# Kernel optimization log

Measured on AMD Instinct MI355X. Metric: run time of the kernel, lower is better.

## Reference

```python
import jax, jax.numpy as jnp
import numpy as np
import math

D_MODEL = 1024
D_HIDDEN = 64
H = 16
B = 2
N = 2048


def softmax_one(x, axis=-1):
    # exp(x - max) / (1 + sum(exp(x - max))) -- matches the torch code exactly
    m = jnp.max(x, axis=axis, keepdims=True)
    e = jnp.exp(x - m)
    return e / (1.0 + jnp.sum(e, axis=axis, keepdims=True))


def setup_inputs() -> dict:
    key = jax.random.key(0)
    ks = jax.random.split(key, 8)
    queries = jax.random.normal(ks[0], (B, N, D_MODEL), dtype=jnp.float32)
    keys = jax.random.normal(ks[1], (B, N, D_MODEL), dtype=jnp.float32)
    values = jax.random.normal(ks[2], (B, N, D_MODEL), dtype=jnp.float32)
    std = 0.02
    Wq = std * jax.random.normal(ks[3], (H * D_HIDDEN, D_MODEL), dtype=jnp.float32)
    Wk = std * jax.random.normal(ks[4], (H * D_HIDDEN, D_MODEL), dtype=jnp.float32)
    Wv = std * jax.random.normal(ks[5], (H * D_HIDDEN, D_MODEL), dtype=jnp.float32)
    Wo = std * jax.random.normal(ks[6], (D_MODEL, H * D_HIDDEN), dtype=jnp.float32)
    bq = jnp.zeros((H * D_HIDDEN,), jnp.float32)
    bk = jnp.zeros((H * D_HIDDEN,), jnp.float32)
    bv = jnp.zeros((H * D_HIDDEN,), jnp.float32)
    bo = jnp.zeros((D_MODEL,), jnp.float32)
    return {"queries": queries, "keys": keys, "values": values,
            "Wq": Wq, "bq": bq, "Wk": Wk, "bk": bk,
            "Wv": Wv, "bv": bv, "Wo": Wo, "bo": bo}


def reference(queries, keys, values, Wq, bq, Wk, bk, Wv, bv, Wo, bo):
    b_s, nq, _ = queries.shape
    nk = keys.shape[1]
    # projections: (b, n, h*dh) -> (b, h, n, dh)
    q = (queries @ Wq.T + bq).reshape(b_s, nq, H, D_HIDDEN).transpose(0, 2, 1, 3)
    k = (keys @ Wk.T + bk).reshape(b_s, nk, H, D_HIDDEN).transpose(0, 2, 1, 3)
    v = (values @ Wv.T + bv).reshape(b_s, nk, H, D_HIDDEN).transpose(0, 2, 1, 3)
    scale = 1.0 / math.sqrt(D_HIDDEN)
    scores = jnp.einsum('bhqd,bhkd->bhqk', q, k) * scale  # (b, h, nq, nk)
    attn = softmax_one(scores, axis=-1)  # dropout disabled (eval)
    out = jnp.einsum('bhqk,bhkd->bhqd', attn, v)  # (b, h, nq, dh)
    out = out.transpose(0, 2, 1, 3).reshape(b_s, nq, H * D_HIDDEN)
    out = out @ Wo.T + bo
    present = jnp.stack((k, v))  # (2, b, h, nk, dh)
    return (out, present)
```

## Files before the change

### kernel.cpp

```cpp
#include <hip/hip_runtime.h>
#include <math.h>

#define D_MODEL 1024
#define DH 64
#define NH 16
#define BS 2
#define SEQ 2048
#define MTOT (BS*SEQ)

typedef _Float16 f16x8 __attribute__((ext_vector_type(8)));
typedef _Float16 f16x4 __attribute__((ext_vector_type(4)));
typedef float f32x4 __attribute__((ext_vector_type(4)));
typedef unsigned int u32;

__device__ __forceinline__ void load_lds16(const void* g, void* l) {
    __builtin_amdgcn_global_load_lds(
        (const __attribute__((address_space(1))) u32*)g,
        (__attribute__((address_space(3))) u32*)l, 16, 0, 0);
}

__global__ __launch_bounds__(256) void convert_all_kernel(
    const float* __restrict__ s0, const float* __restrict__ s1, const float* __restrict__ s2,
    const float* __restrict__ s3, const float* __restrict__ s4, const float* __restrict__ s5,
    const float* __restrict__ s6,
    _Float16* __restrict__ d0, _Float16* __restrict__ d1, _Float16* __restrict__ d2,
    _Float16* __restrict__ d3, _Float16* __restrict__ d4, _Float16* __restrict__ d5,
    _Float16* __restrict__ d6, int nX, int nW)
{
    int y = blockIdx.y;
    const float* s; _Float16* d; int n;
    switch (y) {
        case 0: s = s0; d = d0; n = nX; break;
        case 1: s = s1; d = d1; n = nX; break;
        case 2: s = s2; d = d2; n = nX; break;
        case 3: s = s3; d = d3; n = nW; break;
        case 4: s = s4; d = d4; n = nW; break;
        case 5: s = s5; d = d5; n = nW; break;
        default: s = s6; d = d6; n = nW; break;
    }
    int i = (blockIdx.x * 256 + threadIdx.x) * 8;
    if (i < n) {
        float4 a = *(const float4*)(s + i);
        float4 b = *(const float4*)(s + i + 4);
        f16x8 o;
        o[0] = (_Float16)a.x; o[1] = (_Float16)a.y; o[2] = (_Float16)a.z; o[3] = (_Float16)a.w;
        o[4] = (_Float16)b.x; o[5] = (_Float16)b.y; o[6] = (_Float16)b.z; o[7] = (_Float16)b.w;
        *(f16x8*)(d + i) = o;
    }
}

__global__ __launch_bounds__(256) void qkv_proj_kernel(
    const _Float16* __restrict__ Xq, const _Float16* __restrict__ Xk, const _Float16* __restrict__ Xv,
    const _Float16* __restrict__ Wq, const _Float16* __restrict__ Wk, const _Float16* __restrict__ Wv,
    const float* __restrict__ bq, const float* __restrict__ bk, const float* __restrict__ bv,
    _Float16* __restrict__ qh, _Float16* __restrict__ kh,
    float* __restrict__ outp)
{
    __shared__ __align__(16) _Float16 ldsA[2][128][32];
    __shared__ __align__(16) _Float16 ldsB[2][128][32];

    const int jb = blockIdx.x >> 5;
    const int ib = blockIdx.x & 31;
    const int id = jb >> 3;
    const int col0 = (jb & 7) << 7;
    const int row0 = ib << 7;

    const _Float16* X  = (id == 0) ? Xq : (id == 1) ? Xk : Xv;
    const _Float16* W  = (id == 0) ? Wq : (id == 1) ? Wk : Wv;
    const float* bias  = (id == 0) ? bq : (id == 1) ? bk : bv;

    const int tid = threadIdx.x;
    const int w = tid >> 6, lane = tid & 63;
    const int quad = lane >> 4, l16 = lane & 15;
    const int wm = (w >> 1) << 6, wn = (w & 1) << 6;

    const int sr4 = lane >> 2;
    const int swz = (sr4 & 3) ^ ((sr4 >> 2) & 3);
    const int sg  = (((lane & 3) ^ swz)) << 3;

    const int rswz = ((quad ^ (l16 & 3) ^ ((l16 >> 2) & 3))) << 3;

    const f32x4 zero = {0.f, 0.f, 0.f, 0.f};
    f32x4 acc[4][4];
#pragma unroll
    for (int i = 0; i < 4; i++)
#pragma unroll
        for (int j = 0; j < 4; j++) acc[i][j] = zero;

#pragma unroll
    for (int i = 0; i < 2; i++) {
        int r = i * 64 + w * 16;
        load_lds16(X + (size_t)(row0 + r + sr4) * D_MODEL + sg, &ldsA[0][r][0]);
        load_lds16(W + (size_t)(col0 + r + sr4) * D_MODEL + sg, &ldsB[0][r][0]);
    }

    for (int t = 0; t < D_MODEL / 32; t++) {
        const int cur = t & 1;

        __builtin_amdgcn_s_barrier();

        if (t + 1 < D_MODEL / 32) {
            const int k1 = (t + 1) << 5;
#pragma unroll
            for (int i = 0; i < 2; i++) {
                int r = i * 64 + w * 16;
                load_lds16(X + (size_t)(row0 + r + sr4) * D_MODEL + k1 + sg, &ldsA[cur ^ 1][r][0]);
                load_lds16(W + (size_t)(col0 + r + sr4) * D_MODEL + k1 + sg, &ldsB[cur ^ 1][r][0]);
            }
            asm volatile("s_waitcnt vmcnt(4)" ::: "memory");
        } else {
            asm volatile("s_waitcnt vmcnt(0)" ::: "memory");
        }

        __builtin_amdgcn_s_barrier();

        f16x8 af[4], bfr[4];
#pragma unroll
        for (int mi = 0; mi < 4; mi++)
            af[mi]  = *(const f16x8*)&ldsA[cur][wm + mi*16 + l16][rswz];
#pragma unroll
        for (int ni = 0; ni < 4; ni++)
            bfr[ni] = *(const f16x8*)&ldsB[cur][wn + ni*16 + l16][rswz];
#pragma unroll
        for (int mi = 0; mi < 4; mi++)
#pragma unroll
            for (int ni = 0; ni < 4; ni++)
                acc[mi][ni] = __builtin_amdgcn_mfma_f32_16x16x32_f16(af[mi], bfr[ni], acc[mi][ni], 0, 0, 0);
    }

    const size_t OUT0 = (size_t)MTOT * D_MODEL;
    const size_t PRES = (size_t)BS * NH * SEQ * DH;
#pragma unroll
    for (int ni = 0; ni < 4; ni++) {
        int gn = col0 + wn + ni * 16 + l16;
        float bias_v = bias[gn];
        int h = gn >> 6, d = gn & 63;
#pragma unroll
        for (int mi = 0; mi < 4; mi++) {
#pragma unroll
            for (int r = 0; r < 4; r++) {
                int gm = row0 + wm + mi * 16 + quad * 4 + r;
                float val = acc[mi][ni][r] + bias_v;
                int b = gm >> 11, n = gm & 2047;
                size_t bh = (size_t)(b * NH + h);
                size_t idx = (bh * SEQ + n) * DH + d;
                if (id == 0) {
                    qh[idx] = (_Float16)val;
                } else if (id == 1) {
                    outp[OUT0 + idx] = val;
                    kh[idx] = (_Float16)val;
                } else {
                    outp[OUT0 + PRES + idx] = val;
                }
            }
        }
    }
}

__global__ __launch_bounds__(256) void vtrans_kernel(
    const float* __restrict__ p1, _Float16* __restrict__ vt)
{
    const int bh = blockIdx.x >> 6, nt = blockIdx.x & 63;
    const int tid = threadIdx.x;
    const int d = tid & 63, n8 = tid >> 6;
    const int n0 = nt * 32 + n8 * 8;
    const int tb = n0 & ~63;
    const int p0 = n0 & 63;
    const float* src = p1 + ((size_t)bh * SEQ + tb) * DH + d;
    f16x8 o;
#pragma unroll
    for (int i = 0; i < 8; i++) {
        int p = p0 + i;
        int k = ((p & 0x30) >> 2) | ((p & 0x0C) << 2) | (p & 3);
        o[i] = (_Float16)src[(size_t)k * DH];
    }
    *(f16x8*)(vt + ((size_t)bh * DH + d) * SEQ + n0) = o;
}

__global__ __launch_bounds__(512) void attn_kernel(
    const _Float16* __restrict__ qh, const _Float16* __restrict__ kh,
    const _Float16* __restrict__ vt, _Float16* __restrict__ aout)
{
    __shared__ __align__(16) _Float16 Kt[2][64][76];
    __shared__ __align__(16) _Float16 Vt[2][64][76];

    const int bh = blockIdx.x & 31;
    const int qt = blockIdx.x >> 5;
    const int b = bh >> 4, h = bh & 15;
    const int tid = threadIdx.x;
    const int w = tid >> 6, lane = tid & 63;
    const int quad = lane >> 4, l16 = lane & 15;
    const int qr0 = qt * 128 + w * 16;

    const _Float16* Qb = qh + (size_t)bh * SEQ * DH;
    const _Float16* Kb = kh + (size_t)bh * SEQ * DH;
    const _Float16* Vb = vt + (size_t)bh * DH * SEQ;

    const float QSCALE = 0.125f * 1.44269504f;
    f16x8 aq[2];
#pragma unroll
    for (int ks = 0; ks < 2; ks++) {
        f16x8 t = *(const f16x8*)(Qb + (size_t)(qr0 + l16) * DH + ks * 32 + quad * 8);
#pragma unroll
        for (int j = 0; j < 8; j++) t[j] = (_Float16)((float)t[j] * QSCALE);
        aq[ks] = t;
    }

    const int sr = tid >> 3, sc = (tid & 7) << 3;

    *(f16x8*)&Kt[0][sr][sc] = *(const f16x8*)(Kb + (size_t)sr * DH + sc);
    *(f16x8*)&Vt[0][sr][sc] = *(const f16x8*)(Vb + (size_t)sr * SEQ + sc);
    __syncthreads();

    float m2 = -INFINITY, lsum = 0.f;
    const f32x4 zero = {0.f, 0.f, 0.f, 0.f};
    f32x4 accO[4];
#pragma unroll
    for (int db = 0; db < 4; db++) accO[db] = zero;

    for (int t = 0; t < SEQ / 64; t++) {
        const int cur = t & 1;
        const int kc = t * 64;

        f16x8 kr, vr;
        if (t + 1 < SEQ / 64) {
            kr = *(const f16x8*)(Kb + (size_t)(kc + 64 + sr) * DH + sc);
            vr = *(const f16x8*)(Vb + (size_t)sr * SEQ + kc + 64 + sc);
        }

        f32x4 sT[4];
#pragma unroll
        for (int nb = 0; nb < 4; nb++) sT[nb] = zero;
#pragma unroll
        for (int ks = 0; ks < 2; ks++)
#pragma unroll
            for (int nb = 0; nb < 4; nb++) {
                f16x8 kf = *(const f16x8*)&Kt[cur][nb*16 + l16][ks*32 + quad*8];
                sT[nb] = __builtin_amdgcn_mfma_f32_16x16x32_f16(kf, aq[ks], sT[nb], 0, 0, 0);
            }

        f16x4 pf[4];
        float pmax[4], psum[4];
#pragma unroll
        for (int nb = 0; nb < 4; nb++) {
            float e0 = __builtin_amdgcn_exp2f(sT[nb][0]);
            float e1 = __builtin_amdgcn_exp2f(sT[nb][1]);
            float e2 = __builtin_amdgcn_exp2f(sT[nb][2]);
            float e3 = __builtin_amdgcn_exp2f(sT[nb][3]);
            pf[nb][0] = (_Float16)e0; pf[nb][1] = (_Float16)e1;
            pf[nb][2] = (_Float16)e2; pf[nb][3] = (_Float16)e3;
            psum[nb] = (e0 + e1) + (e2 + e3);
            pmax[nb] = fmaxf(fmaxf(sT[nb][0], sT[nb][1]), fmaxf(sT[nb][2], sT[nb][3]));
        }
        lsum += (psum[0] + psum[1]) + (psum[2] + psum[3]);
        m2 = fmaxf(m2, fmaxf(fmaxf(pmax[0], pmax[1]), fmaxf(pmax[2], pmax[3])));

#pragma unroll
        for (int db = 0; db < 4; db++) {
            f16x8 v01 = *(const f16x8*)&Vt[cur][db*16 + l16][quad*16];
            f16x8 v23 = *(const f16x8*)&Vt[cur][db*16 + l16][quad*16 + 8];
            f16x4 vf0 = __builtin_shufflevector(v01, v01, 0, 1, 2, 3);
            f16x4 vf1 = __builtin_shufflevector(v01, v01, 4, 5, 6, 7);
            f16x4 vf2 = __builtin_shufflevector(v23, v23, 0, 1, 2, 3);
            f16x4 vf3 = __builtin_shufflevector(v23, v23, 4, 5, 6, 7);
            accO[db] = __builtin_amdgcn_mfma_f32_16x16x16f16(vf0, pf[0], accO[db], 0, 0, 0);
            accO[db] = __builtin_amdgcn_mfma_f32_16x16x16f16(vf1, pf[1], accO[db], 0, 0, 0);
            accO[db] = __builtin_amdgcn_mfma_f32_16x16x16f16(vf2, pf[2], accO[db], 0, 0, 0);
            accO[db] = __builtin_amdgcn_mfma_f32_16x16x16f16(vf3, pf[3], accO[db], 0, 0, 0);
        }

        if (t + 1 < SEQ / 64) {
            *(f16x8*)&Kt[cur ^ 1][sr][sc] = kr;
            *(f16x8*)&Vt[cur ^ 1][sr][sc] = vr;
        }
        __syncthreads();
    }

    m2 = fmaxf(m2, __shfl_xor(m2, 16));
    m2 = fmaxf(m2, __shfl_xor(m2, 32));
    lsum += __shfl_xor(lsum, 16);
    lsum += __shfl_xor(lsum, 32);

    const float inv = 1.f / (__builtin_amdgcn_exp2f(m2) + lsum);
    const int q = qr0 + l16;
    _Float16* orow = aout + ((size_t)b * SEQ + q) * D_MODEL + h * DH + quad * 4;
#pragma unroll
    for (int db = 0; db < 4; db++) {
        f16x4 o;
#pragma unroll
        for (int r = 0; r < 4; r++) o[r] = (_Float16)(accO[db][r] * inv);
        *(f16x4*)(orow + db * 16) = o;
    }
}

__global__ __launch_bounds__(256) void out_proj_kernel(
    const _Float16* __restrict__ aout, const _Float16* __restrict__ Wo,
    const float* __restrict__ bo, float* __restrict__ outp)
{
    __shared__ __align__(16) _Float16 ldsA[2][64][64];
    __shared__ __align__(16) _Float16 ldsB[2][128][64];

    const int jb = blockIdx.x >> 6;
    const int ib = blockIdx.x & 63;
    const int col0 = jb << 7, row0 = ib << 6;
    const int tid = threadIdx.x;
    const int w = tid >> 6, lane = tid & 63;
    const int quad = lane >> 4, l16 = lane & 15;
    const int wm = (w >> 1) << 5, wn = (w & 1) << 6;

    const int r_loc = lane >> 3;
    const int sg = ((lane & 7) ^ r_loc) << 3;

    const f32x4 zero = {0.f, 0.f, 0.f, 0.f};
    f32x4 acc[2][4];
#pragma unroll
    for (int i = 0; i < 2; i++)
#pragma unroll
        for (int j = 0; j < 4; j++) acc[i][j] = zero;

#pragma unroll
    for (int i = 0; i < 2; i++) {
        int r = i * 32 + w * 8;
        load_lds16(aout + (size_t)(row0 + r + r_loc) * D_MODEL + sg, &ldsA[0][r][0]);
    }
#pragma unroll
    for (int i = 0; i < 4; i++) {
        int r = i * 32 + w * 8;
        load_lds16(Wo + (size_t)(col0 + r + r_loc) * D_MODEL + sg, &ldsB[0][r][0]);
    }

    for (int t = 0; t < D_MODEL / 64; t++) {
        const int cur = t & 1;

        __builtin_amdgcn_s_barrier();

        if (t + 1 < D_MODEL / 64) {
            const int k1 = (t + 1) << 6;
#pragma unroll
            for (int i = 0; i < 2; i++) {
                int r = i * 32 + w * 8;
                load_lds16(aout + (size_t)(row0 + r + r_loc) * D_MODEL + k1 + sg, &ldsA[cur ^ 1][r][0]);
            }
#pragma unroll
            for (int i = 0; i < 4; i++) {
                int r = i * 32 + w * 8;
                load_lds16(Wo + (size_t)(col0 + r + r_loc) * D_MODEL + k1 + sg, &ldsB[cur ^ 1][r][0]);
            }
            asm volatile("s_waitcnt vmcnt(6)" ::: "memory");
        } else {
            asm volatile("s_waitcnt vmcnt(0)" ::: "memory");
        }

        __builtin_amdgcn_s_barrier();

#pragma unroll
        for (int kk = 0; kk < 2; kk++) {
            f16x8 af[2], bfr[4];
#pragma unroll
            for (int mi = 0; mi < 2; mi++)
                af[mi]  = *(const f16x8*)&ldsA[cur][wm + mi*16 + l16][(((kk<<2) + quad) ^ (l16 & 7)) << 3];
#pragma unroll
            for (int ni = 0; ni < 4; ni++)
                bfr[ni] = *(const f16x8*)&ldsB[cur][wn + ni*16 + l16][(((kk<<2) + quad) ^ (l16 & 7)) << 3];
#pragma unroll
            for (int mi = 0; mi < 2; mi++)
#pragma unroll
                for (int ni = 0; ni < 4; ni++)
                    acc[mi][ni] = __builtin_amdgcn_mfma_f32_16x16x32_f16(af[mi], bfr[ni], acc[mi][ni], 0, 0, 0);
        }
    }

#pragma unroll
    for (int ni = 0; ni < 4; ni++) {
        int gn = col0 + wn + ni * 16 + l16;
        float bias_v = bo[gn];
#pragma unroll
        for (int mi = 0; mi < 2; mi++)
#pragma unroll
            for (int r = 0; r < 4; r++) {
                int gm = row0 + wm + mi * 16 + quad * 4 + r;
                outp[(size_t)gm * D_MODEL + gn] = acc[mi][ni][r] + bias_v;
            }
    }
}

extern "C" void kernel_launch(void* const* d_in, const int* in_sizes, int n_in,
                              void* d_out, int out_size, void* d_ws, size_t ws_size,
                              hipStream_t stream)
{
    const float* queries = (const float*)d_in[0];
    const float* keys    = (const float*)d_in[1];
    const float* values  = (const float*)d_in[2];
    const float* Wq = (const float*)d_in[3];
    const float* bq = (const float*)d_in[4];
    const float* Wk = (const float*)d_in[5];
    const float* bk = (const float*)d_in[6];
    const float* Wv = (const float*)d_in[7];
    const float* bv = (const float*)d_in[8];
    const float* Wo = (const float*)d_in[9];
    const float* bo = (const float*)d_in[10];
    float* outp = (float*)d_out;

    const size_t NELT = (size_t)BS * NH * SEQ * DH;
    const size_t XN   = (size_t)MTOT * D_MODEL;
    const size_t WN   = (size_t)D_MODEL * D_MODEL;
    _Float16* qh   = (_Float16*)d_ws;
    _Float16* kh   = qh + NELT;
    _Float16* vt   = kh + NELT;
    _Float16* aout = vt + NELT;
    _Float16* Xfq  = aout + NELT;
    _Float16* Xfk  = Xfq + XN;
    _Float16* Xfv  = Xfk + XN;
    _Float16* Wfq  = Xfv + XN;
    _Float16* Wfk  = Wfq + WN;
    _Float16* Wfv  = Wfk + WN;
    _Float16* Wfo  = Wfv + WN;

    const size_t OUT0 = (size_t)MTOT * D_MODEL;
    const size_t PRES = NELT;
    const float* present1 = outp + OUT0 + PRES;

    convert_all_kernel<<<dim3((int)(XN/2048), 7), dim3(256), 0, stream>>>(
        queries, keys, values, Wq, Wk, Wv, Wo,
        Xfq, Xfk, Xfv, Wfq, Wfk, Wfv, Wfo, (int)XN, (int)WN);

    qkv_proj_kernel<<<dim3(768), dim3(256), 0, stream>>>(
        Xfq, Xfk, Xfv, Wfq, Wfk, Wfv, bq, bk, bv, qh, kh, outp);
    vtrans_kernel<<<dim3(2048), dim3(256), 0, stream>>>(present1, vt);
    attn_kernel<<<dim3(512), dim3(512), 0, stream>>>(qh, kh, vt, aout);
    out_proj_kernel<<<dim3(512), dim3(256), 0, stream>>>(aout, Wfo, bo, outp);
}
```

Before: 240.6 us.

## Load K fragments directly from global into registers, double-buffered across iterations

K tiles are no longer staged through shared memory. Each lane loads its MFMA K fragments straight from global memory into two register buffers that alternate across a manually unrolled pair of iterations, so the next tile's load overlaps the current compute. Only V still goes through the LDS double buffer. The P conversion also switches to a packed round-toward-zero f16 convert. The costs are higher register pressure (16 f16x8 K fragments per lane), and every one of the 8 waves now reads the same K data from global/L2 instead of sharing one LDS copy.

```diff
diff --git a/kernel.cpp b/kernel.cpp
--- a/kernel.cpp
+++ b/kernel.cpp
@@ -10,6 +10,7 @@
 
 typedef _Float16 f16x8 __attribute__((ext_vector_type(8)));
 typedef _Float16 f16x4 __attribute__((ext_vector_type(4)));
+typedef _Float16 f16x2 __attribute__((ext_vector_type(2)));
 typedef float f32x4 __attribute__((ext_vector_type(4)));
 typedef unsigned int u32;
 
@@ -181,7 +182,6 @@
     const _Float16* __restrict__ qh, const _Float16* __restrict__ kh,
     const _Float16* __restrict__ vt, _Float16* __restrict__ aout)
 {
-    __shared__ __align__(16) _Float16 Kt[2][64][76];
     __shared__ __align__(16) _Float16 Vt[2][64][76];
 
     const int bh = blockIdx.x & 31;
@@ -207,9 +207,17 @@
     }
 
     const int sr = tid >> 3, sc = (tid & 7) << 3;
-
-    *(f16x8*)&Kt[0][sr][sc] = *(const f16x8*)(Kb + (size_t)sr * DH + sc);
     *(f16x8*)&Vt[0][sr][sc] = *(const f16x8*)(Vb + (size_t)sr * SEQ + sc);
+
+    const _Float16* kp = Kb + (size_t)l16 * DH + quad * 8;
+
+    f16x8 kfA[8], kfB[8];
+#pragma unroll
+    for (int ks = 0; ks < 2; ks++)
+#pragma unroll
+        for (int nb = 0; nb < 4; nb++)
+            kfA[ks * 4 + nb] = *(const f16x8*)(kp + (size_t)(nb * 16) * DH + ks * 32);
+
     __syncthreads();
 
     float m2 = -INFINITY, lsum = 0.f;
@@ -218,63 +226,76 @@
 #pragma unroll
     for (int db = 0; db < 4; db++) accO[db] = zero;
 
-    for (int t = 0; t < SEQ / 64; t++) {
-        const int cur = t & 1;
-        const int kc = t * 64;
-
-        f16x8 kr, vr;
-        if (t + 1 < SEQ / 64) {
-            kr = *(const f16x8*)(Kb + (size_t)(kc + 64 + sr) * DH + sc);
-            vr = *(const f16x8*)(Vb + (size_t)sr * SEQ + kc + 64 + sc);
-        }
-
-        f32x4 sT[4];
-#pragma unroll
-        for (int nb = 0; nb < 4; nb++) sT[nb] = zero;
-#pragma unroll
-        for (int ks = 0; ks < 2; ks++)
-#pragma unroll
-            for (int nb = 0; nb < 4; nb++) {
-                f16x8 kf = *(const f16x8*)&Kt[cur][nb*16 + l16][ks*32 + quad*8];
-                sT[nb] = __builtin_amdgcn_mfma_f32_16x16x32_f16(kf, aq[ks], sT[nb], 0, 0, 0);
-            }
-
-        f16x4 pf[4];
-        float pmax[4], psum[4];
-#pragma unroll
-        for (int nb = 0; nb < 4; nb++) {
-            float e0 = __builtin_amdgcn_exp2f(sT[nb][0]);
-            float e1 = __builtin_amdgcn_exp2f(sT[nb][1]);
-            float e2 = __builtin_amdgcn_exp2f(sT[nb][2]);
-            float e3 = __builtin_amdgcn_exp2f(sT[nb][3]);
-            pf[nb][0] = (_Float16)e0; pf[nb][1] = (_Float16)e1;
-            pf[nb][2] = (_Float16)e2; pf[nb][3] = (_Float16)e3;
-            psum[nb] = (e0 + e1) + (e2 + e3);
-            pmax[nb] = fmaxf(fmaxf(sT[nb][0], sT[nb][1]), fmaxf(sT[nb][2], sT[nb][3]));
-        }
-        lsum += (psum[0] + psum[1]) + (psum[2] + psum[3]);
-        m2 = fmaxf(m2, fmaxf(fmaxf(pmax[0], pmax[1]), fmaxf(pmax[2], pmax[3])));
-
-#pragma unroll
-        for (int db = 0; db < 4; db++) {
-            f16x8 v01 = *(const f16x8*)&Vt[cur][db*16 + l16][quad*16];
-            f16x8 v23 = *(const f16x8*)&Vt[cur][db*16 + l16][quad*16 + 8];
-            f16x4 vf0 = __builtin_shufflevector(v01, v01, 0, 1, 2, 3);
-            f16x4 vf1 = __builtin_shufflevector(v01, v01, 4, 5, 6, 7);
-            f16x4 vf2 = __builtin_shufflevector(v23, v23, 0, 1, 2, 3);
-            f16x4 vf3 = __builtin_shufflevector(v23, v23, 4, 5, 6, 7);
-            accO[db] = __builtin_amdgcn_mfma_f32_16x16x16f16(vf0, pf[0], accO[db], 0, 0, 0);
-            accO[db] = __builtin_amdgcn_mfma_f32_16x16x16f16(vf1, pf[1], accO[db], 0, 0, 0);
-            accO[db] = __builtin_amdgcn_mfma_f32_16x16x16f16(vf2, pf[2], accO[db], 0, 0, 0);
-            accO[db] = __builtin_amdgcn_mfma_f32_16x16x16f16(vf3, pf[3], accO[db], 0, 0, 0);
-        }
-
-        if (t + 1 < SEQ / 64) {
-            *(f16x8*)&Kt[cur ^ 1][sr][sc] = kr;
-            *(f16x8*)&Vt[cur ^ 1][sr][sc] = vr;
-        }
-        __syncthreads();
-    }
+#define ATTN_ITER(T, CUR, KF_CUR, KF_NXT)                                      \
+    {                                                                          \
+        const int kc = (T) * 64;                                               \
+        const bool more = (T) + 1 < SEQ / 64;                                  \
+        f16x8 vr;                                                              \
+        if (more)                                                              \
+            vr = *(const f16x8*)(Vb + (size_t)sr * SEQ + kc + 64 + sc);        \
+                    \
+        f32x4 sT[4];                                                           \
+        _Pragma("unroll")                                                      \
+        for (int nb = 0; nb < 4; nb++) sT[nb] = zero;                          \
+        _Pragma("unroll")                                                      \
+        for (int ks = 0; ks < 2; ks++)                                         \
+            _Pragma("unroll")                                                  \
+            for (int nb = 0; nb < 4; nb++)                                     \
+                sT[nb] = __builtin_amdgcn_mfma_f32_16x16x32_f16(               \
+                    KF_CUR[ks * 4 + nb], aq[ks], sT[nb], 0, 0, 0);             \
+         \
+        if (more) {                                                            \
+            const _Float16* kpt = kp + (size_t)(kc + 64) * DH;                 \
+            _Pragma("unroll")                                                  \
+            for (int ks = 0; ks < 2; ks++)                                     \
+                _Pragma("unroll")                                              \
+                for (int nb = 0; nb < 4; nb++)                                 \
+                    KF_NXT[ks * 4 + nb] =                                      \
+                        *(const f16x8*)(kpt + (size_t)(nb * 16) * DH + ks * 32); \
+        }                                                                      \
+                 \
+        f16x4 pf[4];                                                           \
+        float pmax[4], psum[4];                                                \
+        _Pragma("unroll")                                                      \
+        for (int nb = 0; nb < 4; nb++) {                                       \
+            float e0 = __builtin_amdgcn_exp2f(sT[nb][0]);                      \
+            float e1 = __builtin_amdgcn_exp2f(sT[nb][1]);                      \
+            float e2 = __builtin_amdgcn_exp2f(sT[nb][2]);                      \
+            float e3 = __builtin_amdgcn_exp2f(sT[nb][3]);                      \
+            f16x2 plo = __builtin_bit_cast(f16x2, __builtin_amdgcn_cvt_pkrtz(e0, e1)); \
+            f16x2 phi = __builtin_bit_cast(f16x2, __builtin_amdgcn_cvt_pkrtz(e2, e3)); \
+            pf[nb] = __builtin_shufflevector(plo, phi, 0, 1, 2, 3);            \
+            psum[nb] = (e0 + e1) + (e2 + e3);                                  \
+            pmax[nb] = fmaxf(fmaxf(sT[nb][0], sT[nb][1]),                      \
+                             fmaxf(sT[nb][2], sT[nb][3]));                     \
+        }                                                                      \
+        lsum += (psum[0] + psum[1]) + (psum[2] + psum[3]);                     \
+        m2 = fmaxf(m2, fmaxf(fmaxf(pmax[0], pmax[1]),                          \
+                             fmaxf(pmax[2], pmax[3])));                        \
+           \
+        _Pragma("unroll")                                                      \
+        for (int db = 0; db < 4; db++) {                                       \
+            f16x8 v01 = *(const f16x8*)&Vt[CUR][db * 16 + l16][quad * 16];     \
+            f16x8 v23 = *(const f16x8*)&Vt[CUR][db * 16 + l16][quad * 16 + 8]; \
+            f16x4 vf0 = __builtin_shufflevector(v01, v01, 0, 1, 2, 3);         \
+            f16x4 vf1 = __builtin_shufflevector(v01, v01, 4, 5, 6, 7);         \
+            f16x4 vf2 = __builtin_shufflevector(v23, v23, 0, 1, 2, 3);         \
+            f16x4 vf3 = __builtin_shufflevector(v23, v23, 4, 5, 6, 7);         \
+            accO[db] = __builtin_amdgcn_mfma_f32_16x16x16f16(vf0, pf[0], accO[db], 0, 0, 0); \
+            accO[db] = __builtin_amdgcn_mfma_f32_16x16x16f16(vf1, pf[1], accO[db], 0, 0, 0); \
+            accO[db] = __builtin_amdgcn_mfma_f32_16x16x16f16(vf2, pf[2], accO[db], 0, 0, 0); \
+            accO[db] = __builtin_amdgcn_mfma_f32_16x16x16f16(vf3, pf[3], accO[db], 0, 0, 0); \
+        }                                                                      \
+        if (more)                                                              \
+            *(f16x8*)&Vt[(CUR) ^ 1][sr][sc] = vr;                              \
+        __syncthreads();                                                       \
+    }
+
+    for (int tt = 0; tt < SEQ / 128; tt++) {
+        ATTN_ITER(2 * tt,     0, kfA, kfB)
+        ATTN_ITER(2 * tt + 1, 1, kfB, kfA)
+    }
+#undef ATTN_ITER
 
     m2 = fmaxf(m2, __shfl_xor(m2, 16));
     m2 = fmaxf(m2, __shfl_xor(m2, 32));
```

Measured after the change: 312.2 us. 29.8% more time.

## Fuse fp32-to-fp16 activation conversion into QKV projection LDS load

Applied to the files above, without the earlier changes.

The separate pass that converted the three fp32 activation tensors to fp16 is removed. The QKV projection now streams fp32 activation tiles directly into LDS with a new XOR swizzle and converts them to fp16 in registers before the MFMA. This saves writing and rereading about 24MB of fp16 copies. In exchange, each activation tile is reloaded by the 8 column blocks in fp32, doubling global and LDS traffic for A, and the loop now pays extra LDS footprint and conversion instructions.

```diff
diff --git a/kernel.cpp b/kernel.cpp
--- a/kernel.cpp
+++ b/kernel.cpp
@@ -19,24 +19,19 @@
         (__attribute__((address_space(3))) u32*)l, 16, 0, 0);
 }
 
-__global__ __launch_bounds__(256) void convert_all_kernel(
-    const float* __restrict__ s0, const float* __restrict__ s1, const float* __restrict__ s2,
-    const float* __restrict__ s3, const float* __restrict__ s4, const float* __restrict__ s5,
-    const float* __restrict__ s6,
-    _Float16* __restrict__ d0, _Float16* __restrict__ d1, _Float16* __restrict__ d2,
-    _Float16* __restrict__ d3, _Float16* __restrict__ d4, _Float16* __restrict__ d5,
-    _Float16* __restrict__ d6, int nX, int nW)
+__global__ __launch_bounds__(256) void convert_w_kernel(
+    const float* __restrict__ s0, const float* __restrict__ s1,
+    const float* __restrict__ s2, const float* __restrict__ s3,
+    _Float16* __restrict__ d0, _Float16* __restrict__ d1,
+    _Float16* __restrict__ d2, _Float16* __restrict__ d3, int n)
 {
     int y = blockIdx.y;
-    const float* s; _Float16* d; int n;
+    const float* s; _Float16* d;
     switch (y) {
-        case 0: s = s0; d = d0; n = nX; break;
-        case 1: s = s1; d = d1; n = nX; break;
-        case 2: s = s2; d = d2; n = nX; break;
-        case 3: s = s3; d = d3; n = nW; break;
-        case 4: s = s4; d = d4; n = nW; break;
-        case 5: s = s5; d = d5; n = nW; break;
-        default: s = s6; d = d6; n = nW; break;
+        case 0: s = s0; d = d0; break;
+        case 1: s = s1; d = d1; break;
+        case 2: s = s2; d = d2; break;
+        default: s = s3; d = d3; break;
     }
     int i = (blockIdx.x * 256 + threadIdx.x) * 8;
     if (i < n) {
@@ -50,13 +45,13 @@
 }
 
 __global__ __launch_bounds__(256) void qkv_proj_kernel(
-    const _Float16* __restrict__ Xq, const _Float16* __restrict__ Xk, const _Float16* __restrict__ Xv,
+    const float* __restrict__ Xq, const float* __restrict__ Xk, const float* __restrict__ Xv,
     const _Float16* __restrict__ Wq, const _Float16* __restrict__ Wk, const _Float16* __restrict__ Wv,
     const float* __restrict__ bq, const float* __restrict__ bk, const float* __restrict__ bv,
     _Float16* __restrict__ qh, _Float16* __restrict__ kh,
     float* __restrict__ outp)
 {
-    __shared__ __align__(16) _Float16 ldsA[2][128][32];
+    __shared__ __align__(16) float    ldsA[2][128][32];
     __shared__ __align__(16) _Float16 ldsB[2][128][32];
 
     const int jb = blockIdx.x >> 5;
@@ -65,20 +60,23 @@
     const int col0 = (jb & 7) << 7;
     const int row0 = ib << 7;
 
-    const _Float16* X  = (id == 0) ? Xq : (id == 1) ? Xk : Xv;
-    const _Float16* W  = (id == 0) ? Wq : (id == 1) ? Wk : Wv;
-    const float* bias  = (id == 0) ? bq : (id == 1) ? bk : bv;
+    const float*     X = (id == 0) ? Xq : (id == 1) ? Xk : Xv;
+    const _Float16*  W = (id == 0) ? Wq : (id == 1) ? Wk : Wv;
+    const float*  bias = (id == 0) ? bq : (id == 1) ? bk : bv;
 
     const int tid = threadIdx.x;
     const int w = tid >> 6, lane = tid & 63;
     const int quad = lane >> 4, l16 = lane & 15;
     const int wm = (w >> 1) << 6, wn = (w & 1) << 6;
 
+    const int sr8 = lane >> 3;
+    const int sgA = ((lane & 7) ^ sr8) << 2;
+
     const int sr4 = lane >> 2;
-    const int swz = (sr4 & 3) ^ ((sr4 >> 2) & 3);
-    const int sg  = (((lane & 3) ^ swz)) << 3;
-
-    const int rswz = ((quad ^ (l16 & 3) ^ ((l16 >> 2) & 3))) << 3;
+    const int swzB = (sr4 & 3) ^ ((sr4 >> 2) & 3);
+    const int sgB  = ((lane & 3) ^ swzB) << 3;
+
+    const int rswzB = ((quad ^ (l16 & 3) ^ ((l16 >> 2) & 3))) << 3;
 
     const f32x4 zero = {0.f, 0.f, 0.f, 0.f};
     f32x4 acc[4][4];
@@ -88,10 +86,14 @@
         for (int j = 0; j < 4; j++) acc[i][j] = zero;
 
 #pragma unroll
+    for (int i = 0; i < 4; i++) {
+        int r = i * 32 + w * 8;
+        load_lds16(X + (size_t)(row0 + r + sr8) * D_MODEL + sgA, &ldsA[0][r][0]);
+    }
+#pragma unroll
     for (int i = 0; i < 2; i++) {
         int r = i * 64 + w * 16;
-        load_lds16(X + (size_t)(row0 + r + sr4) * D_MODEL + sg, &ldsA[0][r][0]);
-        load_lds16(W + (size_t)(col0 + r + sr4) * D_MODEL + sg, &ldsB[0][r][0]);
+        load_lds16(W + (size_t)(col0 + r + sr4) * D_MODEL + sgB, &ldsB[0][r][0]);
     }
 
     for (int t = 0; t < D_MODEL / 32; t++) {
@@ -102,12 +104,16 @@
         if (t + 1 < D_MODEL / 32) {
             const int k1 = (t + 1) << 5;
 #pragma unroll
+            for (int i = 0; i < 4; i++) {
+                int r = i * 32 + w * 8;
+                load_lds16(X + (size_t)(row0 + r + sr8) * D_MODEL + k1 + sgA, &ldsA[cur ^ 1][r][0]);
+            }
+#pragma unroll
             for (int i = 0; i < 2; i++) {
                 int r = i * 64 + w * 16;
-                load_lds16(X + (size_t)(row0 + r + sr4) * D_MODEL + k1 + sg, &ldsA[cur ^ 1][r][0]);
-                load_lds16(W + (size_t)(col0 + r + sr4) * D_MODEL + k1 + sg, &ldsB[cur ^ 1][r][0]);
-            }
-            asm volatile("s_waitcnt vmcnt(4)" ::: "memory");
+                load_lds16(W + (size_t)(col0 + r + sr4) * D_MODEL + k1 + sgB, &ldsB[cur ^ 1][r][0]);
+            }
+            asm volatile("s_waitcnt vmcnt(6)" ::: "memory");
         } else {
             asm volatile("s_waitcnt vmcnt(0)" ::: "memory");
         }
@@ -116,11 +122,20 @@
 
         f16x8 af[4], bfr[4];
 #pragma unroll
-        for (int mi = 0; mi < 4; mi++)
-            af[mi]  = *(const f16x8*)&ldsA[cur][wm + mi*16 + l16][rswz];
+        for (int mi = 0; mi < 4; mi++) {
+            int row = wm + mi * 16 + l16;
+            f32x4 alo = *(const f32x4*)&ldsA[cur][row][(((quad << 1)    ) ^ (l16 & 7)) << 2];
+            f32x4 ahi = *(const f32x4*)&ldsA[cur][row][(((quad << 1) | 1) ^ (l16 & 7)) << 2];
+            f16x8 a;
+            a[0] = (_Float16)alo[0]; a[1] = (_Float16)alo[1];
+            a[2] = (_Float16)alo[2]; a[3] = (_Float16)alo[3];
+            a[4] = (_Float16)ahi[0]; a[5] = (_Float16)ahi[1];
+            a[6] = (_Float16)ahi[2]; a[7] = (_Float16)ahi[3];
+            af[mi] = a;
+        }
 #pragma unroll
         for (int ni = 0; ni < 4; ni++)
-            bfr[ni] = *(const f16x8*)&ldsB[cur][wn + ni*16 + l16][rswz];
+            bfr[ni] = *(const f16x8*)&ldsB[cur][wn + ni*16 + l16][rswzB];
 #pragma unroll
         for (int mi = 0; mi < 4; mi++)
 #pragma unroll
@@ -402,16 +417,12 @@
     float* outp = (float*)d_out;
 
     const size_t NELT = (size_t)BS * NH * SEQ * DH;
-    const size_t XN   = (size_t)MTOT * D_MODEL;
     const size_t WN   = (size_t)D_MODEL * D_MODEL;
     _Float16* qh   = (_Float16*)d_ws;
     _Float16* kh   = qh + NELT;
     _Float16* vt   = kh + NELT;
     _Float16* aout = vt + NELT;
-    _Float16* Xfq  = aout + NELT;
-    _Float16* Xfk  = Xfq + XN;
-    _Float16* Xfv  = Xfk + XN;
-    _Float16* Wfq  = Xfv + XN;
+    _Float16* Wfq  = aout + NELT;
     _Float16* Wfk  = Wfq + WN;
     _Float16* Wfv  = Wfk + WN;
     _Float16* Wfo  = Wfv + WN;
@@ -420,12 +431,11 @@
     const size_t PRES = NELT;
     const float* present1 = outp + OUT0 + PRES;
 
-    convert_all_kernel<<<dim3((int)(XN/2048), 7), dim3(256), 0, stream>>>(
-        queries, keys, values, Wq, Wk, Wv, Wo,
-        Xfq, Xfk, Xfv, Wfq, Wfk, Wfv, Wfo, (int)XN, (int)WN);
+    convert_w_kernel<<<dim3((int)(WN/2048), 4), dim3(256), 0, stream>>>(
+        Wq, Wk, Wv, Wo, Wfq, Wfk, Wfv, Wfo, (int)WN);
 
     qkv_proj_kernel<<<dim3(768), dim3(256), 0, stream>>>(
-        Xfq, Xfk, Xfv, Wfq, Wfk, Wfv, bq, bk, bv, qh, kh, outp);
+        queries, keys, values, Wfq, Wfk, Wfv, bq, bk, bv, qh, kh, outp);
     vtrans_kernel<<<dim3(2048), dim3(256), 0, stream>>>(present1, vt);
     attn_kernel<<<dim3(512), dim3(512), 0, stream>>>(qh, kh, vt, aout);
     out_proj_kernel<<<dim3(512), dim3(256), 0, stream>>>(aout, Wfo, bo, outp);
```

Measured after the change: 258.5 us. +7.5%, slower.
